# Kernel optimization log

Hardware: AMD Instinct MI355X
Metric: run time of the kernel (lower is better)

The kernel has to match this reference:

```python
import jax, jax.numpy as jnp
import numpy as np

NUM_EMBEDDINGS = 256
EMBEDDING_DIM = 8


def setup_inputs() -> dict:
    key = jax.random.key(0)
    ks = jax.random.split(key, 8)
    B, D_in, H, D_out = 1024, 512, 2048, 512
    s = lambda fan: 1.0 / np.sqrt(fan)
    return {
        "x": jax.random.normal(ks[0], (B, D_in), dtype=jnp.float32),
        "emb_W": jax.random.normal(ks[1], (NUM_EMBEDDINGS, EMBEDDING_DIM), dtype=jnp.float32),
        "W_in": jax.random.normal(ks[2], (H, D_in), dtype=jnp.float32) * s(D_in),
        "b_in": jax.random.normal(ks[3], (H,), dtype=jnp.float32) * s(D_in),
        "W_h": jax.random.normal(ks[4], (H, H), dtype=jnp.float32) * s(H),
        "b_h": jax.random.normal(ks[5], (H,), dtype=jnp.float32) * s(H),
        "W_out": jax.random.normal(ks[6], (D_out, H), dtype=jnp.float32) * s(H),
        "b_out": jax.random.normal(ks[7], (D_out,), dtype=jnp.float32) * s(H),
    }


def reference(x, emb_W, W_in, b_in, W_h, b_h, W_out, b_out):
    B, D_in = x.shape
    flat = x.reshape(-1)  # [B*D_in], row-major flatten == torch .flatten()
    # power-feature expansion: powers 1..embedding_dim stacked on axis 1
    exps = jnp.arange(1, EMBEDDING_DIM + 1, dtype=x.dtype)
    x_res = flat[:, None] ** exps[None, :]  # [B*D_in, E]
    # get_ind: NOTE source uses sum(flat_x) (not sum of squares) -- faithful
    sm = jnp.sum(x_res, axis=1, keepdims=True)              # [N,1]
    emb = jnp.sum(emb_W * emb_W, axis=1)[None, :]           # [1,K]
    dist = sm + emb - 2.0 * (x_res @ emb_W.T)               # [N,K]
    ind = jnp.argmin(dist, axis=1)                          # [N] int
    # q = ind.view_as(x.T).T : reshape to [D_in, B] then transpose
    q = ind.reshape(D_in, B).T.astype(x.dtype)              # [B, D_in]
    # straight-through: forward value q, gradient flows to x
    q = x + jax.lax.stop_gradient(q - x)
    relu = jax.nn.relu
    h = relu(q @ W_in.T + b_in)      # d_in
    for _ in range(4):               # shared d_h applied 4 times
        h = relu(h @ W_h.T + b_h)
    f = relu(h @ W_out.T + b_out)    # d_out
    q_latent_loss = jnp.float32(0.0)  # eval mode
    return (f, q_latent_loss)
```

## Files before the change

kernel.cpp:

```cpp
#include <hip/hip_runtime.h>
#include <hip/hip_bf16.h>
#include <math.h>


#define B_ROWS 1024
#define D_IN   512
#define HDIM   2048
#define NTOT   (B_ROWS * D_IN)
#define NCODE  256
#define EDIM   8

typedef __attribute__((ext_vector_type(8))) short bf16x8;
typedef __attribute__((ext_vector_type(4))) float f32x4;

__device__ inline void gload_lds16(const void* g, void* l) {
    __builtin_amdgcn_global_load_lds(
        (const __attribute__((address_space(1))) void*)g,
        (__attribute__((address_space(3))) void*)l, 16, 0, 0);
}

__device__ inline ushort bf16_hi_bits(float v, float* hi_f) {
    __hip_bfloat16 h = __float2bfloat16(v);
    *hi_f = __bfloat162float(h);
    ushort u; __builtin_memcpy(&u, &h, 2); return u;
}
__device__ inline ushort bf16_bits(float v) {
    __hip_bfloat16 h = __float2bfloat16(v);
    ushort u; __builtin_memcpy(&u, &h, 2); return u;
}

__global__ __launch_bounds__(256) void fused_pre(
    const float* __restrict__ x, const float* __restrict__ embW,
    const float* __restrict__ Wi, const float* __restrict__ Wh,
    ushort* __restrict__ qhi,
    ushort* __restrict__ wihi, ushort* __restrict__ wilo,
    ushort* __restrict__ whhi, ushort* __restrict__ whlo,
    float* __restrict__ loss_out)
{
    __shared__ float sWE[NCODE][12];
    const int tid = threadIdx.x;

    if (blockIdx.x >= 1024) {
        const int sidx = blockIdx.x - 1024;
        #pragma unroll
        for (int s = 0; s < 4; ++s) {
            const int g = sidx * 1024 + s * 256 + tid;
            const float* src; ushort* hi; ushort* lo; int j;
            if (g < 262144) { src = Wi; hi = wihi; lo = wilo; j = g; }
            else            { src = Wh; hi = whhi; lo = whlo; j = g - 262144; }
            float4 v = reinterpret_cast<const float4*>(src)[j];
            float f[4] = {v.x, v.y, v.z, v.w};
            ushort hh[4], ll[4];
            #pragma unroll
            for (int c = 0; c < 4; ++c) {
                float hf;
                hh[c] = bf16_hi_bits(f[c], &hf);
                ll[c] = bf16_bits(f[c] - hf);
            }
            ushort4 h4 = {hh[0], hh[1], hh[2], hh[3]};
            ushort4 l4 = {ll[0], ll[1], ll[2], ll[3]};
            reinterpret_cast<ushort4*>(hi)[j] = h4;
            reinterpret_cast<ushort4*>(lo)[j] = l4;
        }
        return;
    }

    {
        const float4 a4 = *reinterpret_cast<const float4*>(&embW[tid * EDIM]);
        const float4 b4 = *reinterpret_cast<const float4*>(&embW[tid * EDIM + 4]);
        float s0 = __fmul_rn(a4.x, a4.x), s1 = __fmul_rn(a4.y, a4.y);
        float s2 = __fmul_rn(a4.z, a4.z), s3 = __fmul_rn(a4.w, a4.w);
        float s4 = __fmul_rn(b4.x, b4.x), s5 = __fmul_rn(b4.y, b4.y);
        float s6 = __fmul_rn(b4.z, b4.z), s7 = __fmul_rn(b4.w, b4.w);
        float a = __fadd_rn(__fadd_rn(s0, s1), __fadd_rn(s2, s3));
        float b = __fadd_rn(__fadd_rn(s4, s5), __fadd_rn(s6, s7));
        sWE[tid][0] = a4.x; sWE[tid][1] = a4.y; sWE[tid][2] = a4.z; sWE[tid][3] = a4.w;
        sWE[tid][4] = b4.x; sWE[tid][5] = b4.y; sWE[tid][6] = b4.z; sWE[tid][7] = b4.w;
        sWE[tid][8] = __fadd_rn(a, b);
    }
    __syncthreads();

    const int nbase = blockIdx.x * 512 + tid;

    float p2[2][EDIM], sm[2];
    #pragma unroll
    for (int j = 0; j < 2; ++j) {
        const float v = x[nbase + j * 256];
        float p[EDIM];
        #pragma unroll
        for (int e = 0; e < EDIM; ++e)
            p[e] = powf(v, (float)(e + 1));
        float a = __fadd_rn(__fadd_rn(p[0], p[1]), __fadd_rn(p[2], p[3]));
        float b = __fadd_rn(__fadd_rn(p[4], p[5]), __fadd_rn(p[6], p[7]));
        sm[j] = __fadd_rn(a, b);
        #pragma unroll
        for (int e = 0; e < EDIM; ++e)
            p2[j][e] = 2.0f * p[e];
    }

    float best[2] = {INFINITY, INFINITY};
    int   bi[2]   = {0, 0};
    for (int k = 0; k < NCODE; ++k) {
        const float4 w0 = *reinterpret_cast<const float4*>(&sWE[k][0]);
        const float4 w1 = *reinterpret_cast<const float4*>(&sWE[k][4]);
        const float  Ek = sWE[k][8];
        #pragma unroll
        for (int j = 0; j < 2; ++j) {
            float dot = 0.f;
            dot = fmaf(p2[j][0], w0.x, dot); dot = fmaf(p2[j][1], w0.y, dot);
            dot = fmaf(p2[j][2], w0.z, dot); dot = fmaf(p2[j][3], w0.w, dot);
            dot = fmaf(p2[j][4], w1.x, dot); dot = fmaf(p2[j][5], w1.y, dot);
            dot = fmaf(p2[j][6], w1.z, dot); dot = fmaf(p2[j][7], w1.w, dot);
            float d = __fsub_rn(__fadd_rn(sm[j], Ek), dot);
            if (d < best[j]) { best[j] = d; bi[j] = k; }
        }
    }

    #pragma unroll
    for (int j = 0; j < 2; ++j) {
        const int n  = nbase + j * 256;
        const int bo = n & (B_ROWS - 1);
        const int dd = n >> 10;
        qhi[bo * D_IN + dd] = bf16_bits((float)bi[j]);
    }
    if (blockIdx.x == 0 && tid == 0) loss_out[0] = 0.0f;
}

__global__ __launch_bounds__(256) void wo_split(
    const float* __restrict__ Wo, ushort* __restrict__ hi, ushort* __restrict__ lo)
{
    const int tid = threadIdx.x;
    #pragma unroll
    for (int s = 0; s < 4; ++s) {
        const int j = blockIdx.x * 1024 + s * 256 + tid;
        float4 v = reinterpret_cast<const float4*>(Wo)[j];
        float f[4] = {v.x, v.y, v.z, v.w};
        ushort hh[4], ll[4];
        #pragma unroll
        for (int c = 0; c < 4; ++c) {
            float hf;
            hh[c] = bf16_hi_bits(f[c], &hf);
            ll[c] = bf16_bits(f[c] - hf);
        }
        ushort4 h4 = {hh[0], hh[1], hh[2], hh[3]};
        ushort4 l4 = {ll[0], ll[1], ll[2], ll[3]};
        reinterpret_cast<ushort4*>(hi)[j] = h4;
        reinterpret_cast<ushort4*>(lo)[j] = l4;
    }
}

template<bool ALO, bool PARTIAL>
__global__ __launch_bounds__(256) void gemm_split(
    const ushort* __restrict__ Ahi, const ushort* __restrict__ Alo,
    const ushort* __restrict__ Whi, const ushort* __restrict__ Wlo,
    const float* __restrict__ bias,
    ushort* __restrict__ Ohi, ushort* __restrict__ Olo,
    float* __restrict__ OF, int N, int K, int klen)
{
    constexpr int BUF = 49152;
    constexpr int OFF_AH = 0, OFF_AL = 8192, OFF_BH = 16384;
    __shared__ char lds[2 * BUF];

    const int tid = threadIdx.x, lane = tid & 63, wid = tid >> 6;

    const int gy = gridDim.y;
    const int nwg = gridDim.x * gy;
    int lin = blockIdx.x * gy + blockIdx.y;
    int q   = nwg >> 3;
    int sw  = (lin & 7) * q + (lin >> 3);
    int bx  = sw / gy, by2 = sw % gy;
    const int bm   = (by2 & 15) << 6;
    const int kz   = by2 >> 4;
    const int kbeg = kz * klen;
    const int bn   = bx << 7;

    const int wm = (wid >> 1) << 5;
    const int wn = (wid & 1) << 6;

    constexpr int NSEGW = ALO ? 12 : 10;
    const ushort* gp[NSEGW];
    uint ldsoff[NSEGW];
    #pragma unroll
    for (int i = 0; i < NSEGW; ++i) {
        int s = wid + i * 4;
        const ushort* pl; int row0, base, sip;
        if (ALO) {
            if (s < 8)       { pl = Ahi; row0 = bm; base = OFF_AH;         sip = s; }
            else if (s < 16) { pl = Alo; row0 = bm; base = OFF_AL;         sip = s - 8; }
            else if (s < 32) { pl = Whi; row0 = bn; base = OFF_BH;         sip = s - 16; }
            else             { pl = Wlo; row0 = bn; base = OFF_BH + 16384; sip = s - 32; }
        } else {
            if (s < 8)       { pl = Ahi; row0 = bm; base = OFF_AH;         sip = s; }
            else if (s < 24) { pl = Whi; row0 = bn; base = OFF_BH;         sip = s - 8; }
            else             { pl = Wlo; row0 = bn; base = OFF_BH + 16384; sip = s - 24; }
        }
        int r  = sip * 8 + (lane >> 3);
        int ch = (lane & 7) ^ (r & 7);
        gp[i]     = pl + (size_t)(row0 + r) * K + kbeg + ch * 8;
        ldsoff[i] = base + sip * 1024;
    }

    uint aoff[2][2], boff[4][2];
    #pragma unroll
    for (int f = 0; f < 2; ++f) {
        int ar = wm + f * 16 + (lane & 15);
        #pragma unroll
        for (int s = 0; s < 2; ++s) {
            int ch = (s * 4 + (lane >> 4)) ^ (ar & 7);
            aoff[f][s] = OFF_AH + ar * 128 + ch * 16;
        }
    }
    #pragma unroll
    for (int f = 0; f < 4; ++f) {
        int br = wn + f * 16 + (lane & 15);
        #pragma unroll
        for (int s = 0; s < 2; ++s) {
            int ch = (s * 4 + (lane >> 4)) ^ (br & 7);
            boff[f][s] = OFF_BH + br * 128 + ch * 16;
        }
    }

    auto stage = [&](int kt, int b) {
        #pragma unroll
        for (int i = 0; i < NSEGW; ++i)
            gload_lds16(gp[i] + kt * 64, lds + b * BUF + ldsoff[i]);
    };

    f32x4 acc[2][4] = {};
    const int NT = klen >> 6;

    stage(0, 0);
    __syncthreads();

    for (int t = 0; t < NT; ++t) {
        const int cur = t & 1;
        if (t + 1 < NT) stage(t + 1, cur ^ 1);

        const char* lb = lds + cur * BUF;
        bf16x8 aH[2][2], aL[2][2], bH[2][4], bL[2][4];
        #pragma unroll
        for (int s = 0; s < 2; ++s) {
            #pragma unroll
            for (int f = 0; f < 2; ++f) {
                aH[s][f] = *(const bf16x8*)(lb + aoff[f][s]);
                if constexpr (ALO) aL[s][f] = *(const bf16x8*)(lb + aoff[f][s] + 8192);
            }
            #pragma unroll
            for (int f = 0; f < 4; ++f) {
                bH[s][f] = *(const bf16x8*)(lb + boff[f][s]);
                bL[s][f] = *(const bf16x8*)(lb + boff[f][s] + 16384);
            }
        }
        #pragma unroll
        for (int s = 0; s < 2; ++s) {
            #pragma unroll
            for (int fm = 0; fm < 2; ++fm)
                #pragma unroll
                for (int fn = 0; fn < 4; ++fn)
                    acc[fm][fn] = __builtin_amdgcn_mfma_f32_16x16x32_bf16(
                        aH[s][fm], bH[s][fn], acc[fm][fn], 0, 0, 0);
            #pragma unroll
            for (int fm = 0; fm < 2; ++fm)
                #pragma unroll
                for (int fn = 0; fn < 4; ++fn)
                    acc[fm][fn] = __builtin_amdgcn_mfma_f32_16x16x32_bf16(
                        aH[s][fm], bL[s][fn], acc[fm][fn], 0, 0, 0);
            if constexpr (ALO) {
                #pragma unroll
                for (int fm = 0; fm < 2; ++fm)
                    #pragma unroll
                    for (int fn = 0; fn < 4; ++fn)
                        acc[fm][fn] = __builtin_amdgcn_mfma_f32_16x16x32_bf16(
                            aL[s][fm], bH[s][fn], acc[fm][fn], 0, 0, 0);
            }
        }
        __syncthreads();
    }

    #pragma unroll
    for (int fm = 0; fm < 2; ++fm) {
        #pragma unroll
        for (int fn = 0; fn < 4; ++fn) {
            const int col = bn + wn + fn * 16 + (lane & 15);
            const int rb  = bm + wm + fm * 16 + ((lane >> 4) << 2);
            if constexpr (PARTIAL) {
                #pragma unroll
                for (int r = 0; r < 4; ++r)
                    OF[(size_t)(kz * B_ROWS + rb + r) * N + col] = acc[fm][fn][r];
            } else {
                const float bc = bias[col];
                #pragma unroll
                for (int r = 0; r < 4; ++r) {
                    float v = acc[fm][fn][r] + bc;
                    v = v > 0.f ? v : 0.f;
                    float hf;
                    ushort hb = bf16_hi_bits(v, &hf);
                    Ohi[(size_t)(rb + r) * N + col] = hb;
                    Olo[(size_t)(rb + r) * N + col] = bf16_bits(v - hf);
                }
            }
        }
    }
}

__global__ __launch_bounds__(256, 3) void gemm_mid(
    const ushort* __restrict__ Ahi, const ushort* __restrict__ Alo,
    const ushort* __restrict__ Bhi, const ushort* __restrict__ Blo,
    float* __restrict__ OF, int N, int Kfull, int klen)
{
    constexpr int BUFSZ = 24576;
    __shared__ char lds[2 * BUFSZ];

    const int tid = threadIdx.x, lane = tid & 63, wid = tid >> 6;

    const int gy = gridDim.y;
    const int nwg = gridDim.x * gy;
    int lin = blockIdx.x * gy + blockIdx.y;
    int q   = nwg >> 3;
    int sw  = (lin & 7) * q + (lin >> 3);
    int bx  = sw / gy, by2 = sw % gy;
    const int bm   = (by2 & 7) << 7;
    const int kz   = by2 >> 3;
    const int kbeg = kz * klen;
    const int bn   = bx << 6;

    const int wm = (wid >> 1) << 6;
    const int wn = (wid & 1) << 5;

    const int r_l = lane >> 2;
    const int chs = (lane & 3) ^ ((r_l >> 1) & 3);
    const ushort* gp[6];
    uint ldsoff[6];
    #pragma unroll
    for (int i = 0; i < 6; ++i) {
        const int s = wid + i * 4;
        const ushort* pl; int row0; uint base;
        if (s < 8)       { pl = Ahi; row0 = bm + s * 16;        base = (uint)s * 1024; }
        else if (s < 16) { pl = Alo; row0 = bm + (s - 8) * 16;  base = 8192  + (uint)(s - 8)  * 1024; }
        else if (s < 20) { pl = Bhi; row0 = bn + (s - 16) * 16; base = 16384 + (uint)(s - 16) * 1024; }
        else             { pl = Blo; row0 = bn + (s - 20) * 16; base = 20480 + (uint)(s - 20) * 1024; }
        gp[i]     = pl + (size_t)(row0 + r_l) * Kfull + kbeg + chs * 8;
        ldsoff[i] = base;
    }

    uint aoff[4], boff[2];
    #pragma unroll
    for (int f = 0; f < 4; ++f) {
        const int ar = wm + f * 16 + (lane & 15);
        aoff[f] = (uint)(ar * 64 + ((((lane >> 4)) ^ ((ar >> 1) & 3)) << 4));
    }
    #pragma unroll
    for (int f = 0; f < 2; ++f) {
        const int br = wn + f * 16 + (lane & 15);
        boff[f] = (uint)(16384 + br * 64 + ((((lane >> 4)) ^ ((br >> 1) & 3)) << 4));
    }

    auto stage = [&](int kt, int b) {
        #pragma unroll
        for (int i = 0; i < 6; ++i)
            gload_lds16(gp[i] + kt * 32, lds + b * BUFSZ + ldsoff[i]);
    };

    f32x4 acc[4][2] = {};
    const int NT = klen >> 5;

    stage(0, 0);
    __syncthreads();

    for (int t = 0; t < NT; ++t) {
        const int cur = t & 1;
        if (t + 1 < NT) stage(t + 1, cur ^ 1);

        const char* lb = lds + cur * BUFSZ;
        bf16x8 aH[4], aL[4], bH[2], bL[2];
        #pragma unroll
        for (int f = 0; f < 4; ++f) {
            aH[f] = *(const bf16x8*)(lb + aoff[f]);
            aL[f] = *(const bf16x8*)(lb + aoff[f] + 8192);
        }
        #pragma unroll
        for (int f = 0; f < 2; ++f) {
            bH[f] = *(const bf16x8*)(lb + boff[f]);
            bL[f] = *(const bf16x8*)(lb + boff[f] + 4096);
        }
        #pragma unroll
        for (int fm = 0; fm < 4; ++fm)
            #pragma unroll
            for (int fn = 0; fn < 2; ++fn)
                acc[fm][fn] = __builtin_amdgcn_mfma_f32_16x16x32_bf16(
                    aH[fm], bH[fn], acc[fm][fn], 0, 0, 0);
        #pragma unroll
        for (int fm = 0; fm < 4; ++fm)
            #pragma unroll
            for (int fn = 0; fn < 2; ++fn)
                acc[fm][fn] = __builtin_amdgcn_mfma_f32_16x16x32_bf16(
                    aH[fm], bL[fn], acc[fm][fn], 0, 0, 0);
        #pragma unroll
        for (int fm = 0; fm < 4; ++fm)
            #pragma unroll
            for (int fn = 0; fn < 2; ++fn)
                acc[fm][fn] = __builtin_amdgcn_mfma_f32_16x16x32_bf16(
                    aL[fm], bH[fn], acc[fm][fn], 0, 0, 0);
        __syncthreads();
    }

    #pragma unroll
    for (int fm = 0; fm < 4; ++fm) {
        #pragma unroll
        for (int fn = 0; fn < 2; ++fn) {
            const int col = bn + wn + fn * 16 + (lane & 15);
            const int rb  = bm + wm + fm * 16 + ((lane >> 4) << 2);
            #pragma unroll
            for (int r = 0; r < 4; ++r)
                OF[(size_t)(kz * B_ROWS + rb + r) * N + col] = acc[fm][fn][r];
        }
    }
}

__global__ __launch_bounds__(256) void combine_mid(
    const float* __restrict__ part, const float* __restrict__ bias,
    ushort* __restrict__ hi, ushort* __restrict__ lo)
{
    const int i = blockIdx.x * 256 + threadIdx.x;
    const float4* p = (const float4*)part;
    float4 a = p[i], b = p[i + 524288];
    float4 bb = ((const float4*)bias)[i & 511];
    float f[4] = {a.x + b.x + bb.x, a.y + b.y + bb.y,
                  a.z + b.z + bb.z, a.w + b.w + bb.w};
    ushort hh[4], ll[4];
    #pragma unroll
    for (int c = 0; c < 4; ++c) {
        float v = f[c] > 0.f ? f[c] : 0.f;
        float hf;
        hh[c] = bf16_hi_bits(v, &hf);
        ll[c] = bf16_bits(v - hf);
    }
    ushort4 h4 = {hh[0], hh[1], hh[2], hh[3]};
    ushort4 l4 = {ll[0], ll[1], ll[2], ll[3]};
    reinterpret_cast<ushort4*>(hi)[i] = h4;
    reinterpret_cast<ushort4*>(lo)[i] = l4;
}

__global__ __launch_bounds__(256) void combine_relu(
    const float* __restrict__ part, const float* __restrict__ bias,
    float* __restrict__ out)
{
    const int i = blockIdx.x * 256 + threadIdx.x;
    const float4* p = (const float4*)part;
    float4 bb = ((const float4*)bias)[i & 127];
    float ox = bb.x, oy = bb.y, oz = bb.z, ow = bb.w;
    #pragma unroll
    for (int z = 0; z < 8; ++z) {
        float4 a = p[i + z * 131072];
        ox += a.x; oy += a.y; oz += a.z; ow += a.w;
    }
    float4 o;
    o.x = ox > 0.f ? ox : 0.f;
    o.y = oy > 0.f ? oy : 0.f;
    o.z = oz > 0.f ? oz : 0.f;
    o.w = ow > 0.f ? ow : 0.f;
    reinterpret_cast<float4*>(out)[i] = o;
}

extern "C" void kernel_launch(void* const* d_in, const int* in_sizes, int n_in,
                              void* d_out, int out_size, void* d_ws, size_t ws_size,
                              hipStream_t stream)
{
    const float* x     = (const float*)d_in[0];
    const float* emb_W = (const float*)d_in[1];
    const float* W_in  = (const float*)d_in[2];
    const float* b_in  = (const float*)d_in[3];
    const float* W_h   = (const float*)d_in[4];
    const float* b_h   = (const float*)d_in[5];
    const float* W_out = (const float*)d_in[6];
    const float* b_out = (const float*)d_in[7];
    float* out = (float*)d_out;

    char* w = (char*)d_ws;
    const size_t MB = 1 << 20;
    ushort* qhi    = (ushort*)(w);
    ushort* wihi   = (ushort*)(w + 1*MB);
    ushort* wilo   = (ushort*)(w + 3*MB);
    float*  midpar = (float*)(w);
    ushort* wohi   = (ushort*)(w);
    ushort* wolo   = (ushort*)(w + 2*MB);
    ushort* hhi    = (ushort*)(w + 16*MB);
    ushort* hlo    = (ushort*)(w + 20*MB);
    ushort* whhi   = (ushort*)(w + 24*MB);
    ushort* whlo   = (ushort*)(w + 32*MB);
    float*  l6par  = (float*)(w + 24*MB);

    fused_pre<<<2304, 256, 0, stream>>>(x, emb_W, W_in, W_h,
                                        qhi, wihi, wilo, whhi, whlo, out + NTOT);

    gemm_split<false, false><<<dim3(16, 16), 256, 0, stream>>>(
        qhi, nullptr, wihi, wilo, b_in, hhi, hlo, nullptr, HDIM, D_IN, D_IN);

    for (int l = 0; l < 4; ++l) {
        gemm_mid<<<dim3(32, 16), 256, 0, stream>>>(
            hhi, hlo, whhi, whlo, midpar, HDIM, HDIM, 1024);
        combine_mid<<<2048, 256, 0, stream>>>(midpar, b_h, hhi, hlo);
    }

    wo_split<<<256, 256, 0, stream>>>(W_out, wohi, wolo);

    gemm_mid<<<dim3(8, 64), 256, 0, stream>>>(
        hhi, hlo, wohi, wolo, l6par, D_IN, HDIM, 256);

    combine_relu<<<512, 256, 0, stream>>>(l6par, b_out, out);
}
```

Measured before the change: 236.8 us.

## Widen gemm_mid N-tile to 256 and pack VQ distance math into v_pk ops

The mid GEMM's N tile grows from 64 to 256 columns per workgroup. That raises data reuse of the A tile (both hi and lo parts) and cuts the grid from 512 to 128 workgroups for the hidden layers, and from 512 to 128 for the output layer. LDS rises to 96KB and the occupancy hint is dropped, and the accumulators grow to 32 f32x4 per thread. The risks are register pressure and too few workgroups to fill the GPU. Separately, the codebook argmin kernel now handles 4 elements per thread and uses packed f32 FMA via inline asm on duplicated codebook entries in LDS, with branchless min tracking.

```diff
diff --git a/kernel.cpp b/kernel.cpp
--- a/kernel.cpp
+++ b/kernel.cpp
@@ -12,6 +12,7 @@
 
 typedef __attribute__((ext_vector_type(8))) short bf16x8;
 typedef __attribute__((ext_vector_type(4))) float f32x4;
+typedef __attribute__((ext_vector_type(2))) float f32x2;
 
 __device__ inline void gload_lds16(const void* g, void* l) {
     __builtin_amdgcn_global_load_lds(
@@ -37,11 +38,11 @@
     ushort* __restrict__ whhi, ushort* __restrict__ whlo,
     float* __restrict__ loss_out)
 {
-    __shared__ float sWE[NCODE][12];
+    __shared__ float sD[NCODE][20];
     const int tid = threadIdx.x;
 
-    if (blockIdx.x >= 1024) {
-        const int sidx = blockIdx.x - 1024;
+    if (blockIdx.x >= 512) {
+        const int sidx = blockIdx.x - 512;
         #pragma unroll
         for (int s = 0; s < 4; ++s) {
             const int g = sidx * 1024 + s * 256 + tid;
@@ -74,17 +75,21 @@
         float s6 = __fmul_rn(b4.z, b4.z), s7 = __fmul_rn(b4.w, b4.w);
         float a = __fadd_rn(__fadd_rn(s0, s1), __fadd_rn(s2, s3));
         float b = __fadd_rn(__fadd_rn(s4, s5), __fadd_rn(s6, s7));
-        sWE[tid][0] = a4.x; sWE[tid][1] = a4.y; sWE[tid][2] = a4.z; sWE[tid][3] = a4.w;
-        sWE[tid][4] = b4.x; sWE[tid][5] = b4.y; sWE[tid][6] = b4.z; sWE[tid][7] = b4.w;
-        sWE[tid][8] = __fadd_rn(a, b);
+        float E = __fadd_rn(a, b);
+        float* r = sD[tid];
+        r[0]  = a4.x; r[1]  = a4.x; r[2]  = a4.y; r[3]  = a4.y;
+        r[4]  = a4.z; r[5]  = a4.z; r[6]  = a4.w; r[7]  = a4.w;
+        r[8]  = b4.x; r[9]  = b4.x; r[10] = b4.y; r[11] = b4.y;
+        r[12] = b4.z; r[13] = b4.z; r[14] = b4.w; r[15] = b4.w;
+        r[16] = E;    r[17] = E;
     }
     __syncthreads();
 
-    const int nbase = blockIdx.x * 512 + tid;
-
-    float p2[2][EDIM], sm[2];
-    #pragma unroll
-    for (int j = 0; j < 2; ++j) {
+    const int nbase = blockIdx.x * 1024 + tid;
+
+    float p2a[4][EDIM], sm[4];
+    #pragma unroll
+    for (int j = 0; j < 4; ++j) {
         const float v = x[nbase + j * 256];
         float p[EDIM];
         #pragma unroll
@@ -95,33 +100,64 @@
         sm[j] = __fadd_rn(a, b);
         #pragma unroll
         for (int e = 0; e < EDIM; ++e)
-            p2[j][e] = 2.0f * p[e];
-    }
-
-    float best[2] = {INFINITY, INFINITY};
-    int   bi[2]   = {0, 0};
+            p2a[j][e] = 2.0f * p[e];
+    }
+
+    f32x2 pA[EDIM], pB[EDIM];
+    #pragma unroll
+    for (int e = 0; e < EDIM; ++e) {
+        pA[e].x = p2a[0][e]; pA[e].y = p2a[1][e];
+        pB[e].x = p2a[2][e]; pB[e].y = p2a[3][e];
+    }
+    f32x2 smA; smA.x = sm[0]; smA.y = sm[1];
+    f32x2 smB; smB.x = sm[2]; smB.y = sm[3];
+    f32x2 neg1; neg1.x = -1.0f; neg1.y = -1.0f;
+
+    float best[4] = {INFINITY, INFINITY, INFINITY, INFINITY};
+    int   bi[4]   = {0, 0, 0, 0};
+
+    #pragma unroll 2
     for (int k = 0; k < NCODE; ++k) {
-        const float4 w0 = *reinterpret_cast<const float4*>(&sWE[k][0]);
-        const float4 w1 = *reinterpret_cast<const float4*>(&sWE[k][4]);
-        const float  Ek = sWE[k][8];
-        #pragma unroll
-        for (int j = 0; j < 2; ++j) {
-            float dot = 0.f;
-            dot = fmaf(p2[j][0], w0.x, dot); dot = fmaf(p2[j][1], w0.y, dot);
-            dot = fmaf(p2[j][2], w0.z, dot); dot = fmaf(p2[j][3], w0.w, dot);
-            dot = fmaf(p2[j][4], w1.x, dot); dot = fmaf(p2[j][5], w1.y, dot);
-            dot = fmaf(p2[j][6], w1.z, dot); dot = fmaf(p2[j][7], w1.w, dot);
-            float d = __fsub_rn(__fadd_rn(sm[j], Ek), dot);
-            if (d < best[j]) { best[j] = d; bi[j] = k; }
-        }
-    }
-
-    #pragma unroll
-    for (int j = 0; j < 2; ++j) {
-        const int n  = nbase + j * 256;
-        const int bo = n & (B_ROWS - 1);
-        const int dd = n >> 10;
-        qhi[bo * D_IN + dd] = bf16_bits((float)bi[j]);
+        const f32x2* r2 = reinterpret_cast<const f32x2*>(sD[k]);
+        f32x2 w0 = r2[0], w1 = r2[1], w2 = r2[2], w3 = r2[3];
+        f32x2 w4 = r2[4], w5 = r2[5], w6 = r2[6], w7 = r2[7];
+        f32x2 ek = r2[8];
+
+        f32x2 dA, dB;
+        asm("v_pk_mul_f32 %0, %1, %2"     : "=v"(dA) : "v"(pA[0]), "v"(w0));
+        asm("v_pk_mul_f32 %0, %1, %2"     : "=v"(dB) : "v"(pB[0]), "v"(w0));
+        asm("v_pk_fma_f32 %0, %1, %2, %0" : "+v"(dA) : "v"(pA[1]), "v"(w1));
+        asm("v_pk_fma_f32 %0, %1, %2, %0" : "+v"(dB) : "v"(pB[1]), "v"(w1));
+        asm("v_pk_fma_f32 %0, %1, %2, %0" : "+v"(dA) : "v"(pA[2]), "v"(w2));
+        asm("v_pk_fma_f32 %0, %1, %2, %0" : "+v"(dB) : "v"(pB[2]), "v"(w2));
+        asm("v_pk_fma_f32 %0, %1, %2, %0" : "+v"(dA) : "v"(pA[3]), "v"(w3));
+        asm("v_pk_fma_f32 %0, %1, %2, %0" : "+v"(dB) : "v"(pB[3]), "v"(w3));
+        asm("v_pk_fma_f32 %0, %1, %2, %0" : "+v"(dA) : "v"(pA[4]), "v"(w4));
+        asm("v_pk_fma_f32 %0, %1, %2, %0" : "+v"(dB) : "v"(pB[4]), "v"(w4));
+        asm("v_pk_fma_f32 %0, %1, %2, %0" : "+v"(dA) : "v"(pA[5]), "v"(w5));
+        asm("v_pk_fma_f32 %0, %1, %2, %0" : "+v"(dB) : "v"(pB[5]), "v"(w5));
+        asm("v_pk_fma_f32 %0, %1, %2, %0" : "+v"(dA) : "v"(pA[6]), "v"(w6));
+        asm("v_pk_fma_f32 %0, %1, %2, %0" : "+v"(dB) : "v"(pB[6]), "v"(w6));
+        asm("v_pk_fma_f32 %0, %1, %2, %0" : "+v"(dA) : "v"(pA[7]), "v"(w7));
+        asm("v_pk_fma_f32 %0, %1, %2, %0" : "+v"(dB) : "v"(pB[7]), "v"(w7));
+        f32x2 sA, sB;
+        asm("v_pk_add_f32 %0, %1, %2"     : "=v"(sA) : "v"(smA), "v"(ek));
+        asm("v_pk_add_f32 %0, %1, %2"     : "=v"(sB) : "v"(smB), "v"(ek));
+        f32x2 ddA, ddB;
+        asm("v_pk_fma_f32 %0, %1, %2, %3" : "=v"(ddA) : "v"(dA), "v"(neg1), "v"(sA));
+        asm("v_pk_fma_f32 %0, %1, %2, %3" : "=v"(ddB) : "v"(dB), "v"(neg1), "v"(sB));
+
+        float d0 = ddA.x, d1 = ddA.y, d2 = ddB.x, d3 = ddB.y;
+        bi[0] = (d0 < best[0]) ? k : bi[0]; best[0] = fminf(best[0], d0);
+        bi[1] = (d1 < best[1]) ? k : bi[1]; best[1] = fminf(best[1], d1);
+        bi[2] = (d2 < best[2]) ? k : bi[2]; best[2] = fminf(best[2], d2);
+        bi[3] = (d3 < best[3]) ? k : bi[3]; best[3] = fminf(best[3], d3);
+    }
+
+    #pragma unroll
+    for (int j = 0; j < 4; ++j) {
+        const int n = nbase + j * 256;
+        qhi[(n & (B_ROWS - 1)) * D_IN + (n >> 10)] = bf16_bits((float)bi[j]);
     }
     if (blockIdx.x == 0 && tid == 0) loss_out[0] = 0.0f;
 }
@@ -303,13 +339,13 @@
     }
 }
 
-__global__ __launch_bounds__(256, 3) void gemm_mid(
+__global__ __launch_bounds__(256) void gemm_mid(
     const ushort* __restrict__ Ahi, const ushort* __restrict__ Alo,
     const ushort* __restrict__ Bhi, const ushort* __restrict__ Blo,
     float* __restrict__ OF, int N, int Kfull, int klen)
 {
-    constexpr int BUFSZ = 24576;
-    __shared__ char lds[2 * BUFSZ];
+    constexpr int BUF = 49152;
+    __shared__ char lds[2 * BUF];
 
     const int tid = threadIdx.x, lane = tid & 63, wid = tid >> 6;
 
@@ -322,46 +358,46 @@
     const int bm   = (by2 & 7) << 7;
     const int kz   = by2 >> 3;
     const int kbeg = kz * klen;
-    const int bn   = bx << 6;
+    const int bn   = bx << 8;
 
     const int wm = (wid >> 1) << 6;
-    const int wn = (wid & 1) << 5;
+    const int wn = (wid & 1) << 7;
 
     const int r_l = lane >> 2;
     const int chs = (lane & 3) ^ ((r_l >> 1) & 3);
-    const ushort* gp[6];
-    uint ldsoff[6];
-    #pragma unroll
-    for (int i = 0; i < 6; ++i) {
+    const ushort* gp[12];
+    uint ldsoff[12];
+    #pragma unroll
+    for (int i = 0; i < 12; ++i) {
         const int s = wid + i * 4;
         const ushort* pl; int row0; uint base;
         if (s < 8)       { pl = Ahi; row0 = bm + s * 16;        base = (uint)s * 1024; }
         else if (s < 16) { pl = Alo; row0 = bm + (s - 8) * 16;  base = 8192  + (uint)(s - 8)  * 1024; }
-        else if (s < 20) { pl = Bhi; row0 = bn + (s - 16) * 16; base = 16384 + (uint)(s - 16) * 1024; }
-        else             { pl = Blo; row0 = bn + (s - 20) * 16; base = 20480 + (uint)(s - 20) * 1024; }
+        else if (s < 32) { pl = Bhi; row0 = bn + (s - 16) * 16; base = 16384 + (uint)(s - 16) * 1024; }
+        else             { pl = Blo; row0 = bn + (s - 32) * 16; base = 32768 + (uint)(s - 32) * 1024; }
         gp[i]     = pl + (size_t)(row0 + r_l) * Kfull + kbeg + chs * 8;
         ldsoff[i] = base;
     }
 
-    uint aoff[4], boff[2];
+    uint aoff[4], boff[8];
     #pragma unroll
     for (int f = 0; f < 4; ++f) {
         const int ar = wm + f * 16 + (lane & 15);
         aoff[f] = (uint)(ar * 64 + ((((lane >> 4)) ^ ((ar >> 1) & 3)) << 4));
     }
     #pragma unroll
-    for (int f = 0; f < 2; ++f) {
+    for (int f = 0; f < 8; ++f) {
         const int br = wn + f * 16 + (lane & 15);
         boff[f] = (uint)(16384 + br * 64 + ((((lane >> 4)) ^ ((br >> 1) & 3)) << 4));
     }
 
     auto stage = [&](int kt, int b) {
         #pragma unroll
-        for (int i = 0; i < 6; ++i)
-            gload_lds16(gp[i] + kt * 32, lds + b * BUFSZ + ldsoff[i]);
+        for (int i = 0; i < 12; ++i)
+            gload_lds16(gp[i] + kt * 32, lds + b * BUF + ldsoff[i]);
     };
 
-    f32x4 acc[4][2] = {};
+    f32x4 acc[4][8] = {};
     const int NT = klen >> 5;
 
     stage(0, 0);
@@ -371,43 +407,47 @@
         const int cur = t & 1;
         if (t + 1 < NT) stage(t + 1, cur ^ 1);
 
-        const char* lb = lds + cur * BUFSZ;
-        bf16x8 aH[4], aL[4], bH[2], bL[2];
-        #pragma unroll
-        for (int f = 0; f < 4; ++f) {
-            aH[f] = *(const bf16x8*)(lb + aoff[f]);
-            aL[f] = *(const bf16x8*)(lb + aoff[f] + 8192);
-        }
-        #pragma unroll
-        for (int f = 0; f < 2; ++f) {
-            bH[f] = *(const bf16x8*)(lb + boff[f]);
-            bL[f] = *(const bf16x8*)(lb + boff[f] + 4096);
-        }
+        const char* lb = lds + cur * BUF;
+        bf16x8 aH[4], bH[8];
+        #pragma unroll
+        for (int f = 0; f < 4; ++f) aH[f] = *(const bf16x8*)(lb + aoff[f]);
+        #pragma unroll
+        for (int f = 0; f < 8; ++f) bH[f] = *(const bf16x8*)(lb + boff[f]);
         #pragma unroll
         for (int fm = 0; fm < 4; ++fm)
             #pragma unroll
-            for (int fn = 0; fn < 2; ++fn)
+            for (int fn = 0; fn < 8; ++fn)
                 acc[fm][fn] = __builtin_amdgcn_mfma_f32_16x16x32_bf16(
                     aH[fm], bH[fn], acc[fm][fn], 0, 0, 0);
-        #pragma unroll
-        for (int fm = 0; fm < 4; ++fm)
-            #pragma unroll
-            for (int fn = 0; fn < 2; ++fn)
-                acc[fm][fn] = __builtin_amdgcn_mfma_f32_16x16x32_bf16(
-                    aH[fm], bL[fn], acc[fm][fn], 0, 0, 0);
-        #pragma unroll
-        for (int fm = 0; fm < 4; ++fm)
-            #pragma unroll
-            for (int fn = 0; fn < 2; ++fn)
-                acc[fm][fn] = __builtin_amdgcn_mfma_f32_16x16x32_bf16(
-                    aL[fm], bH[fn], acc[fm][fn], 0, 0, 0);
+        {
+            bf16x8 aL[4];
+            #pragma unroll
+            for (int f = 0; f < 4; ++f) aL[f] = *(const bf16x8*)(lb + aoff[f] + 8192);
+            #pragma unroll
+            for (int fm = 0; fm < 4; ++fm)
+                #pragma unroll
+                for (int fn = 0; fn < 8; ++fn)
+                    acc[fm][fn] = __builtin_amdgcn_mfma_f32_16x16x32_bf16(
+                        aL[fm], bH[fn], acc[fm][fn], 0, 0, 0);
+        }
+        {
+            bf16x8 bL[8];
+            #pragma unroll
+            for (int f = 0; f < 8; ++f) bL[f] = *(const bf16x8*)(lb + boff[f] + 16384);
+            #pragma unroll
+            for (int fm = 0; fm < 4; ++fm)
+                #pragma unroll
+                for (int fn = 0; fn < 8; ++fn)
+                    acc[fm][fn] = __builtin_amdgcn_mfma_f32_16x16x32_bf16(
+                        aH[fm], bL[fn], acc[fm][fn], 0, 0, 0);
+        }
         __syncthreads();
     }
 
     #pragma unroll
     for (int fm = 0; fm < 4; ++fm) {
         #pragma unroll
-        for (int fn = 0; fn < 2; ++fn) {
+        for (int fn = 0; fn < 8; ++fn) {
             const int col = bn + wn + fn * 16 + (lane & 15);
             const int rb  = bm + wm + fm * 16 + ((lane >> 4) << 2);
             #pragma unroll
@@ -490,21 +530,21 @@
     ushort* whlo   = (ushort*)(w + 32*MB);
     float*  l6par  = (float*)(w + 24*MB);
 
-    fused_pre<<<2304, 256, 0, stream>>>(x, emb_W, W_in, W_h,
+    fused_pre<<<1792, 256, 0, stream>>>(x, emb_W, W_in, W_h,
                                         qhi, wihi, wilo, whhi, whlo, out + NTOT);
 
     gemm_split<false, false><<<dim3(16, 16), 256, 0, stream>>>(
         qhi, nullptr, wihi, wilo, b_in, hhi, hlo, nullptr, HDIM, D_IN, D_IN);
 
     for (int l = 0; l < 4; ++l) {
-        gemm_mid<<<dim3(32, 16), 256, 0, stream>>>(
+        gemm_mid<<<dim3(8, 16), 256, 0, stream>>>(
             hhi, hlo, whhi, whlo, midpar, HDIM, HDIM, 1024);
         combine_mid<<<2048, 256, 0, stream>>>(midpar, b_h, hhi, hlo);
     }
 
     wo_split<<<256, 256, 0, stream>>>(W_out, wohi, wolo);
 
-    gemm_mid<<<dim3(8, 64), 256, 0, stream>>>(
+    gemm_mid<<<dim3(2, 64), 256, 0, stream>>>(
         hhi, hlo, wohi, wolo, l6par, D_IN, HDIM, 256);
 
     combine_relu<<<512, 256, 0, stream>>>(l6par, b_out, out);
```

After: 305.2 us. +28.9%, slower.
